# Optimization experiments

Measured on AMD Instinct MI355X. Metric: run time of the kernel, lower is better.

The kernel has to match this reference:

```python
import jax, jax.numpy as jnp
import numpy as np

D_MODEL = 1024
NUM_HEADS = 16
D_K = D_MODEL // NUM_HEADS
B, T = 2, 2048


def setup_inputs() -> dict:
    key = jax.random.key(0)
    ks = jax.random.split(key, 11)
    s = 1.0 / np.sqrt(D_MODEL)
    inp = {
        "q": jax.random.normal(ks[0], (B, T, D_MODEL), jnp.float32),
        "k": jax.random.normal(ks[1], (B, T, D_MODEL), jnp.float32),
        "v": jax.random.normal(ks[2], (B, T, D_MODEL), jnp.float32),
        "mask": jnp.tril(jnp.ones((1, 1, T, T), jnp.int32)),  # causal
        "wq": jax.random.normal(ks[3], (D_MODEL, D_MODEL), jnp.float32) * s,
        "bq": jnp.zeros((D_MODEL,), jnp.float32),
        "wk": jax.random.normal(ks[4], (D_MODEL, D_MODEL), jnp.float32) * s,
        "bk": jnp.zeros((D_MODEL,), jnp.float32),
        "wv": jax.random.normal(ks[5], (D_MODEL, D_MODEL), jnp.float32) * s,
        "bv": jnp.zeros((D_MODEL,), jnp.float32),
        "wo": jax.random.normal(ks[6], (D_MODEL, D_MODEL), jnp.float32) * s,
        "bo": jnp.zeros((D_MODEL,), jnp.float32),
    }
    return inp


def reference(q, k, v, mask, wq, bq, wk, bk, wv, bv, wo, bo):
    Bq, Tq, _ = q.shape
    Tk = k.shape[1]
    # projections, split into heads: (B, H, T, d_k)
    qh = (q @ wq + bq).reshape(Bq, Tq, NUM_HEADS, D_K).transpose(0, 2, 1, 3)
    kh = (k @ wk + bk).reshape(Bq, Tk, NUM_HEADS, D_K).transpose(0, 2, 1, 3)
    vh = (v @ wv + bv).reshape(Bq, Tk, NUM_HEADS, D_K).transpose(0, 2, 1, 3)
    scores = jnp.einsum("bhqd,bhkd->bhqk", qh, kh) / jnp.sqrt(jnp.float32(D_K))
    scores = jnp.where(mask == 0, jnp.float32(-1e9), scores)
    attn = jax.nn.softmax(scores, axis=-1)
    ctx = jnp.einsum("bhqk,bhkd->bhqd", attn, vh)
    ctx = ctx.transpose(0, 2, 1, 3).reshape(Bq, Tq, D_MODEL)
    return ctx @ wo + bo
```

## Files before the change

kernel.cpp:

```cpp
#include <hip/hip_runtime.h>
#include <hip/hip_bf16.h>

#define DM 1024
#define NH 16
#define DK 64
#define TT 2048
#define BATCH 2

typedef __attribute__((ext_vector_type(8))) short bf16x8;
typedef __attribute__((ext_vector_type(4))) float f32x4;
typedef __attribute__((ext_vector_type(4))) unsigned short u16x4;
typedef unsigned short u16;

__device__ inline u16 f2b(float x){ __hip_bfloat16 h = __float2bfloat16(x); return *reinterpret_cast<u16*>(&h); }

__device__ inline void gl_lds16(const u16* g, u16* l) {
  __builtin_amdgcn_global_load_lds(
      (const __attribute__((address_space(1))) unsigned int*)g,
      (__attribute__((address_space(3))) unsigned int*)l, 16, 0, 0);
}

__global__ __launch_bounds__(256) void prep(const float* __restrict__ q, const float* __restrict__ k,
                                            const float* __restrict__ v,
                                            const float* __restrict__ wq, const float* __restrict__ wk,
                                            const float* __restrict__ wv, const float* __restrict__ wo,
                                            u16* __restrict__ qb, u16* __restrict__ kb,
                                            u16* __restrict__ vb, u16* __restrict__ wt) {
  int z = blockIdx.z;
  if (z < 3) {
    const float* src = z==0 ? q : z==1 ? k : v;
    u16* dst = z==0 ? qb : z==1 ? kb : vb;
    size_t i = ((size_t)blockIdx.x*256 + threadIdx.x)*8;
    f32x4 a = *(const f32x4*)(src+i);
    f32x4 b = *(const f32x4*)(src+i+4);
    union { bf16x8 v8; u16 e[8]; } u;
    #pragma unroll
    for (int j=0;j<4;j++){ u.e[j] = f2b(a[j]); u.e[4+j] = f2b(b[j]); }
    *(bf16x8*)(dst+i) = u.v8;
  } else {
    int bx = blockIdx.x;
    if (bx >= 1024) return;
    __shared__ float tile[32][33];
    const float* src = z==3 ? wq : z==4 ? wk : z==5 ? wv : wo;
    u16* dst = wt + (size_t)(z-3)*DM*DM;
    int bxx = bx & 31, byy = bx >> 5;
    int tx = threadIdx.x & 31, ty = threadIdx.x >> 5;
    int x  = bxx*32 + tx;
    int y0 = byy*32 + ty;
    #pragma unroll
    for (int i=0;i<32;i+=8) tile[ty+i][tx] = src[(size_t)(y0+i)*DM + x];
    __syncthreads();
    int xo = byy*32 + tx;
    int yo = bxx*32 + ty;
    #pragma unroll
    for (int i=0;i<32;i+=8) dst[(size_t)(yo+i)*DM + xo] = f2b(tile[tx][ty+i]);
  }
}

__global__ __launch_bounds__(512, 2) void gemm_qkv(const u16* __restrict__ qb, const u16* __restrict__ kb,
                                                   const u16* __restrict__ vb, const u16* __restrict__ wt,
                                                   const float* __restrict__ bq, const float* __restrict__ bk,
                                                   const float* __restrict__ bv,
                                                   u16* __restrict__ qh, u16* __restrict__ kh,
                                                   u16* __restrict__ vhT) {
  const int bid = blockIdx.x;
  const int swz = (bid & 7)*24 + (bid >> 3);
  const int z  = swz >> 6;
  const int rb = swz & 63;
  const int row0 = (rb >> 2) * 256;
  const int col0 = (rb & 3) * 256;

  const u16* A = z==0 ? qb : z==1 ? kb : vb;
  const u16* W = wt + (size_t)z*DM*DM;
  const float* bias = z==0 ? bq : z==1 ? bk : bv;
  u16* outv = z==0 ? qh : z==1 ? kh : vhT;
  const int mode = (z==2);
  const float oscale = (z==0) ? 0.125f : 1.0f;

  __shared__ __align__(16) u16 As[2][16384];
  __shared__ __align__(16) u16 Bs[2][16384];

  const int tid = threadIdx.x, lane = tid & 63, wid = tid >> 6;
  const int li = lane & 15, quad = lane >> 4, l7 = lane & 7;
  const int wr = wid >> 2, wc = wid & 3;

  int r_[2], gs_[2];
  #pragma unroll
  for (int c=0;c<2;c++){ int idx = tid + c*512; int rr = idx>>3; int gd = idx&7; r_[c]=rr; gs_[c]=gd^(rr&7); }

  auto stage = [&](int op, int t, int hf, int slot){
    const u16* base = op ? W : A;
    const int rowbase = (op ? col0 : row0) + hf*128;
    u16* lb = (op ? Bs[slot] : As[slot]) + hf*8192;
    #pragma unroll
    for (int c=0;c<2;c++){
      gl_lds16(base + (size_t)(rowbase + r_[c])*DM + t*64 + gs_[c]*8,
               lb + ((wid*64 + c*512) << 3));
    }
  };

  f32x4 acc[8][4];
  #pragma unroll
  for (int i=0;i<8;i++)
    #pragma unroll
    for (int j=0;j<4;j++) acc[i][j] = f32x4{0.f,0.f,0.f,0.f};

  stage(1, 0, 0, 0); stage(1, 0, 1, 0);
  stage(0, 0, 0, 0); stage(0, 0, 1, 0);
  stage(1, 1, 0, 1); stage(1, 1, 1, 1);
  asm volatile("s_waitcnt vmcnt(4)" ::: "memory");
  __builtin_amdgcn_s_barrier();

  bf16x8 b[4][2];
  for (int i = 0; i < 8; i++) {
    const int t2 = 2*i;
    #pragma unroll
    for (int half = 0; half < 2; half++) {
      const int slot = half;
      #pragma unroll
      for (int q = 0; q < 4; q++) {
        if (q == 0) {
          const u16* bb = Bs[slot] + (wc>>1)*8192 + (wc&1)*4096;
          #pragma unroll
          for (int c=0;c<4;c++)
            #pragma unroll
            for (int kh=0;kh<2;kh++)
              b[c][kh] = *(const bf16x8*)&bb[(c*16 + li)*64 + ((quad + 4*kh) ^ l7)*8];
        }
        bf16x8 a[2][2];
        {
          const u16* ab = As[slot] + wr*8192;
          #pragma unroll
          for (int rr2=0; rr2<2; rr2++)
            #pragma unroll
            for (int kh=0;kh<2;kh++)
              a[rr2][kh] = *(const bf16x8*)&ab[((q*2+rr2)*16 + li)*64 + ((quad + 4*kh) ^ l7)*8];
        }
        {
          const int sop = (q >= 2);
          const int st  = t2 + 1 + half + (q >= 2);
          const int shf = q & 1;
          const int ssl = (q >= 2) ? half : (1 - half);
          if (st <= 15) stage(sop, st, shf, ssl);
        }
        if (q == 0) asm volatile("s_waitcnt lgkmcnt(8)" ::: "memory");
        __builtin_amdgcn_s_barrier();
        asm volatile("s_waitcnt lgkmcnt(0)" ::: "memory");
        __builtin_amdgcn_sched_barrier(0);
        __builtin_amdgcn_s_setprio(1);
        #pragma unroll
        for (int rr2=0; rr2<2; rr2++)
          #pragma unroll
          for (int c=0;c<4;c++)
            #pragma unroll
            for (int kh=0;kh<2;kh++)
              acc[q*2+rr2][c] = __builtin_amdgcn_mfma_f32_16x16x32_bf16(a[rr2][kh], b[c][kh], acc[q*2+rr2][c], 0,0,0);
        __builtin_amdgcn_s_setprio(0);
        if (q == 3) {
          if (half == 0) {
            if (i < 7) asm volatile("s_waitcnt vmcnt(4)" ::: "memory");
            else       asm volatile("s_waitcnt vmcnt(0)" ::: "memory");
          } else {
            if (i < 7) asm volatile("s_waitcnt vmcnt(4)" ::: "memory");
          }
        }
        __builtin_amdgcn_s_barrier();
      }
    }
  }

  if (!mode) {
    #pragma unroll
    for (int c=0;c<4;c++) {
      int col = col0 + wc*64 + c*16 + li;
      float bsv = bias[col];
      #pragma unroll
      for (int fr=0; fr<8; fr++) {
        int rowb = row0 + wr*128 + fr*16 + quad*4;
        #pragma unroll
        for (int r=0;r<4;r++)
          outv[(size_t)(rowb + r)*DM + col] = f2b((acc[fr][c][r] + bsv) * oscale);
      }
    }
  } else {
    #pragma unroll
    for (int c=0;c<4;c++) {
      int col = col0 + wc*64 + c*16 + li;
      float bsv = bias[col];
      int hh = col >> 6, d = col & 63;
      #pragma unroll
      for (int fr=0; fr<8; fr++) {
        int rowb = row0 + wr*128 + fr*16 + quad*4;
        int bb = rowb >> 11, t0 = rowb & (TT-1);
        u16x4 w;
        #pragma unroll
        for (int r=0;r<4;r++) w[r] = f2b(acc[fr][c][r] + bsv);
        *(u16x4*)&outv[(((size_t)(bb*NH + hh)*DK + d)*TT) + t0] = w;
      }
    }
  }
}

__global__ __launch_bounds__(256) void gemm_out64(const u16* __restrict__ A, const u16* __restrict__ W,
                                                  const float* __restrict__ bias, float* __restrict__ out) {
  __shared__ __align__(16) u16 As[3][128*32];
  __shared__ __align__(16) u16 Bs[3][64*32];
  const int tid = threadIdx.x, lane = tid & 63, wid = tid >> 6;
  const int li = lane & 15, quad = lane >> 4;
  const int row0 = blockIdx.x*128, col0 = blockIdx.y*64;
  const int wr = wid & 1, wc = wid >> 1;

  const int srow = lane >> 2;
  const int scol = ((lane & 3) ^ ((srow >> 1) & 3)) * 8;
  const int rsw  = (li >> 1) & 3;

  auto stage = [&](int hh, int bufi) {
    const int kk = hh*32;
    #pragma unroll
    for (int c=0;c<2;c++) {
      int ch = wid*2 + c;
      gl_lds16(A + (size_t)(row0 + ch*16 + srow)*DM + kk + scol, &As[bufi][ch*512]);
    }
    gl_lds16(W + (size_t)(col0 + wid*16 + srow)*DM + kk + scol, &Bs[bufi][wid*512]);
  };

  f32x4 acc[4][2];
  #pragma unroll
  for (int i=0;i<4;i++)
    #pragma unroll
    for (int j=0;j<2;j++) acc[i][j] = f32x4{0.f,0.f,0.f,0.f};

  stage(0, 0);
  stage(1, 1);
  asm volatile("s_waitcnt vmcnt(3)" ::: "memory");
  __builtin_amdgcn_s_barrier();

  int buf = 0;
  for (int h = 0; h < 32; h++) {
    bf16x8 a[4], b[2];
    #pragma unroll
    for (int i=0;i<4;i++) a[i] = *(const bf16x8*)&As[buf][(wr*64 + i*16 + li)*32 + (quad ^ rsw)*8];
    #pragma unroll
    for (int j=0;j<2;j++) b[j] = *(const bf16x8*)&Bs[buf][(wc*32 + j*16 + li)*32 + (quad ^ rsw)*8];

    if (h < 30) { int nb = buf + 2; if (nb >= 3) nb -= 3; stage(h+2, nb); }

    __builtin_amdgcn_s_setprio(1);
    #pragma unroll
    for (int i=0;i<4;i++)
      #pragma unroll
      for (int j=0;j<2;j++)
        acc[i][j] = __builtin_amdgcn_mfma_f32_16x16x32_bf16(a[i], b[j], acc[i][j], 0,0,0);
    __builtin_amdgcn_s_setprio(0);

    if (h < 30)       asm volatile("s_waitcnt vmcnt(3)" ::: "memory");
    else if (h == 30) asm volatile("s_waitcnt vmcnt(0)" ::: "memory");
    __builtin_amdgcn_s_barrier();
    if (++buf == 3) buf = 0;
  }

  #pragma unroll
  for (int j=0;j<2;j++) {
    int col = col0 + wc*32 + j*16 + li;
    float bsv = bias[col];
    #pragma unroll
    for (int i=0;i<4;i++) {
      #pragma unroll
      for (int r=0;r<4;r++) {
        int row = row0 + wr*64 + i*16 + quad*4 + r;
        out[(size_t)row*DM + col] = acc[i][j][r] + bsv;
      }
    }
  }
}

__global__ __launch_bounds__(256) void flash(const u16* __restrict__ qh, const u16* __restrict__ kh,
                                             const u16* __restrict__ vhT, u16* __restrict__ ctx) {
  const int bh = blockIdx.x;
  const int qt = 15 - blockIdx.y;
  const int b = bh >> 4, h = bh & 15;
  const u16* Q  = qh  + (size_t)b*TT*DM + h*DK;
  const u16* K  = kh  + (size_t)b*TT*DM + h*DK;
  const u16* Vt = vhT + (size_t)bh*DK*TT;

  const int tid = threadIdx.x, lane = tid & 63, wid = tid >> 6;
  const int li = lane & 15, quad = lane >> 4, l7 = lane & 7;

  __shared__ __align__(16) u16 Kl[64][64];
  __shared__ __align__(16) u16 Vl[64][64];
  __shared__ __align__(16) u16 Pb[4][16][64];

  const int sr = tid >> 3;
  const int sg = tid & 7;
  const int ssl = (sg ^ (sr & 7)) * 8;

  const int nt  = 2*qt + 2;
  const int qw0 = qt*128 + wid*32;

  bf16x8 qf[2][2];
  #pragma unroll
  for (int su=0; su<2; su++)
    #pragma unroll
    for (int k2=0; k2<2; k2++)
      qf[su][k2] = *(const bf16x8*)&Q[(size_t)(qw0 + su*16 + li)*DM + k2*32 + quad*8];

  f32x4 o[2][4];
  #pragma unroll
  for (int su=0; su<2; su++)
    #pragma unroll
    for (int d=0; d<4; d++) o[su][d] = f32x4{0.f,0.f,0.f,0.f};
  float lp[2] = {0.f, 0.f};

  bf16x8 kr0 = *(const bf16x8*)&K[(size_t)(sr   )*DM + sg*8];
  bf16x8 kr1 = *(const bf16x8*)&K[(size_t)(sr+32)*DM + sg*8];
  bf16x8 vr0 = *(const bf16x8*)&Vt[(size_t)(sr   )*TT + sg*8];
  bf16x8 vr1 = *(const bf16x8*)&Vt[(size_t)(sr+32)*TT + sg*8];

  for (int it = 0; it < nt; it++) {
    const int k0 = it*64;
    __syncthreads();
    *(bf16x8*)&Kl[sr   ][ssl] = kr0;
    *(bf16x8*)&Kl[sr+32][ssl] = kr1;
    *(bf16x8*)&Vl[sr   ][ssl] = vr0;
    *(bf16x8*)&Vl[sr+32][ssl] = vr1;
    __syncthreads();
    if (it+1 < nt) {
      const int k1 = k0 + 64;
      kr0 = *(const bf16x8*)&K[(size_t)(k1+sr   )*DM + sg*8];
      kr1 = *(const bf16x8*)&K[(size_t)(k1+sr+32)*DM + sg*8];
      vr0 = *(const bf16x8*)&Vt[(size_t)(sr   )*TT + k1 + sg*8];
      vr1 = *(const bf16x8*)&Vt[(size_t)(sr+32)*TT + k1 + sg*8];
    }

    if (k0 <= qw0 + 31) {
      f32x4 s[2][4];
      __builtin_amdgcn_s_setprio(1);
      #pragma unroll
      for (int c=0;c<4;c++) {
        bf16x8 kf0 = *(const bf16x8*)&Kl[c*16+li][((quad    ) ^ l7)*8];
        bf16x8 kf1 = *(const bf16x8*)&Kl[c*16+li][((quad + 4) ^ l7)*8];
        #pragma unroll
        for (int su=0; su<2; su++) {
          f32x4 t = __builtin_amdgcn_mfma_f32_16x16x32_bf16(kf0, qf[su][0], f32x4{0.f,0.f,0.f,0.f}, 0,0,0);
          s[su][c] = __builtin_amdgcn_mfma_f32_16x16x32_bf16(kf1, qf[su][1], t, 0,0,0);
        }
      }
      __builtin_amdgcn_s_setprio(0);

      bf16x8 vf[4][2];
      #pragma unroll
      for (int d=0; d<4; d++) {
        vf[d][0] = *(const bf16x8*)&Vl[d*16+li][((quad    ) ^ l7)*8];
        vf[d][1] = *(const bf16x8*)&Vl[d*16+li][((quad + 4) ^ l7)*8];
      }

      #pragma unroll
      for (int su=0; su<2; su++) {
        const int qr = qw0 + su*16;
        if (k0 <= qr + 15) {
          const int qq = qr + li;
          float p[4][4];
          if (k0 + 63 > qr) {
            #pragma unroll
            for (int c=0;c<4;c++)
              #pragma unroll
              for (int r=0;r<4;r++){
                int key = k0 + c*16 + quad*4 + r;
                p[c][r] = (key <= qq) ? __expf(s[su][c][r]) : 0.f;
              }
          } else {
            #pragma unroll
            for (int c=0;c<4;c++)
              #pragma unroll
              for (int r=0;r<4;r++)
                p[c][r] = __expf(s[su][c][r]);
          }
          #pragma unroll
          for (int c=0;c<4;c++)
            #pragma unroll
            for (int r=0;r<4;r++)
              lp[su] += p[c][r];

          #pragma unroll
          for (int c=0;c<4;c++) {
            u16x4 w;
            #pragma unroll
            for (int r=0;r<4;r++) w[r] = f2b(p[c][r]);
            const int gc = c*2 + (quad>>1);
            *(u16x4*)&Pb[wid][li][((gc ^ l7)*8) + (quad&1)*4] = w;
          }
          __builtin_amdgcn_wave_barrier();
          __asm__ __volatile__("s_waitcnt lgkmcnt(0)");
          bf16x8 pf0 = *(const bf16x8*)&Pb[wid][li][((quad    ) ^ l7)*8];
          bf16x8 pf1 = *(const bf16x8*)&Pb[wid][li][((quad + 4) ^ l7)*8];

          __builtin_amdgcn_s_setprio(1);
          #pragma unroll
          for (int d=0;d<4;d++){
            o[su][d] = __builtin_amdgcn_mfma_f32_16x16x32_bf16(vf[d][0], pf0, o[su][d], 0,0,0);
            o[su][d] = __builtin_amdgcn_mfma_f32_16x16x32_bf16(vf[d][1], pf1, o[su][d], 0,0,0);
          }
          __builtin_amdgcn_s_setprio(0);
        }
      }
    }
  }

  #pragma unroll
  for (int su=0; su<2; su++) {
    float lpv = lp[su];
    lpv += __shfl_xor(lpv, 16, 64);
    lpv += __shfl_xor(lpv, 32, 64);
    float rl = 1.0f / lpv;
    const int qq = qw0 + su*16 + li;
    #pragma unroll
    for (int d=0;d<4;d++){
      u16x4 w;
      #pragma unroll
      for (int r=0;r<4;r++) w[r] = f2b(o[su][d][r] * rl);
      *(u16x4*)&ctx[(size_t)(b*TT + qq)*DM + h*DK + d*16 + quad*4] = w;
    }
  }
}

extern "C" void kernel_launch(void* const* d_in, const int* in_sizes, int n_in,
                              void* d_out, int out_size, void* d_ws, size_t ws_size,
                              hipStream_t stream) {
  const float* q   = (const float*)d_in[0];
  const float* k   = (const float*)d_in[1];
  const float* v   = (const float*)d_in[2];
  const float* wq  = (const float*)d_in[4];
  const float* bq  = (const float*)d_in[5];
  const float* wk  = (const float*)d_in[6];
  const float* bk  = (const float*)d_in[7];
  const float* wv  = (const float*)d_in[8];
  const float* bv  = (const float*)d_in[9];
  const float* wo  = (const float*)d_in[10];
  const float* bo  = (const float*)d_in[11];
  float* out = (float*)d_out;

  const size_t SZ = (size_t)BATCH*TT*DM;
  u16* wt  = (u16*)d_ws;
  u16* qb  = wt + (size_t)4*DM*DM;
  u16* kb  = qb + SZ;
  u16* vb  = kb + SZ;
  u16* qh  = vb + SZ;
  u16* kh  = qh + SZ;
  u16* vhT = kh + SZ;
  u16* ctx = qb;

  prep<<<dim3(2048, 1, 7), 256, 0, stream>>>(q, k, v, wq, wk, wv, wo, qb, kb, vb, wt);

  gemm_qkv<<<dim3(192, 1, 1), 512, 0, stream>>>(qb, kb, vb, wt, bq, bk, bv, qh, kh, vhT);

  flash<<<dim3(BATCH*NH, 16), 256, 0, stream>>>(qh, kh, vhT, ctx);

  gemm_out64<<<dim3(4096/128, DM/64), 256, 0, stream>>>(ctx, wt + (size_t)3*DM*DM, bo, out);
}
```

Baseline: 224.6 us.

## Double-buffer K/V LDS tiles and interleave heavy and light causal query tiles

The flash kernel now keeps two LDS buffers for the K and V tiles, which removes one of the two block barriers per key iteration. It also changes the mapping from blockIdx.y to query tile so that the first eight launched blocks take the heaviest causal tiles and the rest take the lightest. The intent is less barrier stall time and better load balance across CUs. In exchange, LDS use per block grows, which can lower occupancy, and the launch order changes which tiles run together.

```diff
diff --git a/kernel.cpp b/kernel.cpp
--- a/kernel.cpp
+++ b/kernel.cpp
@@ -277,7 +277,8 @@
 __global__ __launch_bounds__(256) void flash(const u16* __restrict__ qh, const u16* __restrict__ kh,
                                              const u16* __restrict__ vhT, u16* __restrict__ ctx) {
   const int bh = blockIdx.x;
-  const int qt = 15 - blockIdx.y;
+  const int y  = blockIdx.y;
+  const int qt = (y < 8) ? (15 - y) : (y - 8);
   const int b = bh >> 4, h = bh & 15;
   const u16* Q  = qh  + (size_t)b*TT*DM + h*DK;
   const u16* K  = kh  + (size_t)b*TT*DM + h*DK;
@@ -286,8 +287,8 @@
   const int tid = threadIdx.x, lane = tid & 63, wid = tid >> 6;
   const int li = lane & 15, quad = lane >> 4, l7 = lane & 7;
 
-  __shared__ __align__(16) u16 Kl[64][64];
-  __shared__ __align__(16) u16 Vl[64][64];
+  __shared__ __align__(16) u16 Kl[2][64][64];
+  __shared__ __align__(16) u16 Vl[2][64][64];
   __shared__ __align__(16) u16 Pb[4][16][64];
 
   const int sr = tid >> 3;
@@ -318,11 +319,11 @@
 
   for (int it = 0; it < nt; it++) {
     const int k0 = it*64;
-    __syncthreads();
-    *(bf16x8*)&Kl[sr   ][ssl] = kr0;
-    *(bf16x8*)&Kl[sr+32][ssl] = kr1;
-    *(bf16x8*)&Vl[sr   ][ssl] = vr0;
-    *(bf16x8*)&Vl[sr+32][ssl] = vr1;
+    const int s = it & 1;
+    *(bf16x8*)&Kl[s][sr   ][ssl] = kr0;
+    *(bf16x8*)&Kl[s][sr+32][ssl] = kr1;
+    *(bf16x8*)&Vl[s][sr   ][ssl] = vr0;
+    *(bf16x8*)&Vl[s][sr+32][ssl] = vr1;
     __syncthreads();
     if (it+1 < nt) {
       const int k1 = k0 + 64;
@@ -333,16 +334,16 @@
     }
 
     if (k0 <= qw0 + 31) {
-      f32x4 s[2][4];
+      f32x4 sacc[2][4];
       __builtin_amdgcn_s_setprio(1);
       #pragma unroll
       for (int c=0;c<4;c++) {
-        bf16x8 kf0 = *(const bf16x8*)&Kl[c*16+li][((quad    ) ^ l7)*8];
-        bf16x8 kf1 = *(const bf16x8*)&Kl[c*16+li][((quad + 4) ^ l7)*8];
+        bf16x8 kf0 = *(const bf16x8*)&Kl[s][c*16+li][((quad    ) ^ l7)*8];
+        bf16x8 kf1 = *(const bf16x8*)&Kl[s][c*16+li][((quad + 4) ^ l7)*8];
         #pragma unroll
         for (int su=0; su<2; su++) {
           f32x4 t = __builtin_amdgcn_mfma_f32_16x16x32_bf16(kf0, qf[su][0], f32x4{0.f,0.f,0.f,0.f}, 0,0,0);
-          s[su][c] = __builtin_amdgcn_mfma_f32_16x16x32_bf16(kf1, qf[su][1], t, 0,0,0);
+          sacc[su][c] = __builtin_amdgcn_mfma_f32_16x16x32_bf16(kf1, qf[su][1], t, 0,0,0);
         }
       }
       __builtin_amdgcn_s_setprio(0);
@@ -350,8 +351,8 @@
       bf16x8 vf[4][2];
       #pragma unroll
       for (int d=0; d<4; d++) {
-        vf[d][0] = *(const bf16x8*)&Vl[d*16+li][((quad    ) ^ l7)*8];
-        vf[d][1] = *(const bf16x8*)&Vl[d*16+li][((quad + 4) ^ l7)*8];
+        vf[d][0] = *(const bf16x8*)&Vl[s][d*16+li][((quad    ) ^ l7)*8];
+        vf[d][1] = *(const bf16x8*)&Vl[s][d*16+li][((quad + 4) ^ l7)*8];
       }
 
       #pragma unroll
@@ -366,14 +367,14 @@
               #pragma unroll
               for (int r=0;r<4;r++){
                 int key = k0 + c*16 + quad*4 + r;
-                p[c][r] = (key <= qq) ? __expf(s[su][c][r]) : 0.f;
+                p[c][r] = (key <= qq) ? __expf(sacc[su][c][r]) : 0.f;
               }
           } else {
             #pragma unroll
             for (int c=0;c<4;c++)
               #pragma unroll
               for (int r=0;r<4;r++)
-                p[c][r] = __expf(s[su][c][r]);
+                p[c][r] = __expf(sacc[su][c][r]);
           }
           #pragma unroll
           for (int c=0;c<4;c++)
```

Measured after the change: 225.1 us. No clear change (+0.2%).
